# Performance work log

Hardware: AMD Instinct MI355X
Metric: run time of the kernel (lower is better)

Reference implementation:

```python
import jax, jax.numpy as jnp
import numpy as np

B, T, D = 32, 2000, 512
L_ORDER, R_ORDER = 20, 20
L_STRIDE, R_STRIDE = 2, 2
LPAD = L_ORDER * L_STRIDE  # 40
RPAD = R_ORDER * R_STRIDE  # 40


def setup_inputs() -> dict:
    key = jax.random.key(0)
    k1, k2 = jax.random.split(key)
    x = jax.random.normal(k1, (B, T, D), dtype=jnp.float32)
    filt = jax.random.normal(k2, (L_ORDER + R_ORDER + 1, D), dtype=jnp.float32)
    return {"x": x, "filt": filt}


def _fsmn(x, filt):
    # x: [B, T, D], filt: [L_ORDER + R_ORDER + 1, D]
    t = x.shape[1]
    xp = jnp.pad(x, ((0, 0), (LPAD, RPAD), (0, 0)))
    # Center of output frame t sits at padded index t + LPAD.
    # Left tap i hits padded offset t + i*L_STRIDE  (i = 0..L_ORDER-1),
    # i.e. signal offset -(L_ORDER - i)*L_STRIDE relative to the frame.
    out = xp[:, LPAD:LPAD + t] * filt[L_ORDER]  # center tap
    for i in range(L_ORDER):
        s = i * L_STRIDE
        out = out + xp[:, s:s + t] * filt[i]
    # Right tap j hits signal offset 1 + j*R_STRIDE (matches x[f+1 : f+1+R*rs : rs]).
    for j in range(R_ORDER):
        s = LPAD + 1 + j * R_STRIDE
        out = out + xp[:, s:s + t] * filt[L_ORDER + 1 + j]
    return out


def reference(x, filt):
    return _fsmn(x, filt)
```

## Files before the change

### kernel.cpp

```cpp
#include <hip/hip_runtime.h>


#define B_ 32
#define T_ 2000
#define D_ 512
#define S_ 1000
#define M_ 4

#define FOFF 0
#define XOFF (41 * 256)
#define LDS_FLOATS (XOFF + 64 * 256)

__device__ __forceinline__ float4 zf4() {
    float4 z; z.x = 0.f; z.y = 0.f; z.z = 0.f; z.w = 0.f; return z;
}

__device__ __forceinline__ void fma4(float4& a, const float4 f, const float4 w) {
    a.x = fmaf(f.x, w.x, a.x);
    a.y = fmaf(f.y, w.y, a.y);
    a.z = fmaf(f.z, w.z, a.z);
    a.w = fmaf(f.w, w.w, a.w);
}

__device__ __forceinline__ void gload_lds16(const float* g, float* l) {
    __builtin_amdgcn_global_load_lds(
        (const __attribute__((address_space(1))) void*)g,
        (__attribute__((address_space(3))) void*)l,
        16, 0, 0);
}

template<bool CHK>
__device__ __forceinline__ void fsmn_body(float* __restrict__ lds,
                                          const float* __restrict__ xb,
                                          const float* __restrict__ fb,
                                          float* __restrict__ ob,
                                          int m0, int R0, int lane, int mg)
{
    auto stageX = [&](int br) {
        float* l = lds + XOFF + ((br & 63) << 8);
        const int xr = R0 + br;
        if (!CHK || (unsigned)xr < (unsigned)T_) {
            gload_lds16(xb + (size_t)xr * D_, l);
        } else {
            *(float4*)(l + lane * 4) = zf4();
        }
    };
    auto stageF = [&](int fr) {
        gload_lds16(fb + (size_t)fr * D_, lds + FOFF + (fr << 8));
    };
    auto ldrow = [&](int br) -> float4 {
        return *(const float4*)(lds + XOFF + ((br & 63) << 8) + lane * 4);
    };
    auto ldsF = [&](int t) -> float4 {
        return *(const float4*)(lds + FOFF + (t << 8) + lane * 4);
    };

#pragma unroll
    for (int r = 0; r < 11; ++r) {
        const int fr = 4 * r + mg;
        if (fr <= 40) stageF(fr);
    }
#pragma unroll
    for (int r = 0; r < 12; ++r) stageX(4 * r + mg);
    __syncthreads();

    float4 wE[M_], wO[M_], ae[M_], ao[M_];
#pragma unroll
    for (int m = 0; m < M_; ++m) {
        wE[m] = ldrow(8 * mg + 2 * m);
        wO[m] = ldrow(8 * mg + 2 * m + 1);
        ae[m] = zf4(); ao[m] = zf4();
    }
    float4 qF0 = ldsF(0), qF1 = ldsF(1);

    auto dostep = [&](int t) {
        const float4 fv = qF0;
        qF0 = qF1;
        qF1 = (t + 2 <= 40) ? ldsF(t + 2) : zf4();
        if (t <= 20) {
#pragma unroll
            for (int m = 0; m < M_; ++m) { fma4(ae[m], fv, wE[m]); fma4(ao[m], fv, wO[m]); }
        } else {
#pragma unroll
            for (int m = 0; m < M_; ++m) { fma4(ao[m], fv, wE[m]); fma4(ae[m], fv, wO[m]); }
        }
        if (t < 40) {
#pragma unroll
            for (int m = 0; m < M_ - 1; ++m) wE[m] = wE[m + 1];
            wE[M_ - 1] = ldrow(8 * mg + 2 * t + 8);
            if (t != 20) {
#pragma unroll
                for (int m = 0; m < M_ - 1; ++m) wO[m] = wO[m + 1];
                wO[M_ - 1] = ldrow(8 * mg + 2 * t + 8 + ((t < 20) ? 1 : -1));
            }
        }
    };

#pragma unroll
    for (int p = 0; p < 5; ++p) {
        if (p <= 3) {
#pragma unroll
            for (int r = 0; r < 4; ++r) stageX(16 * (p + 3) + 4 * r + mg);
        }
#pragma unroll
        for (int t = 8 * p; t < ((p == 4) ? 41 : 8 * p + 8); ++t) dostep(t);
        if (p < 4) __syncthreads();
    }

#pragma unroll
    for (int m = 0; m < M_; ++m) {
        if (!CHK || (m0 + m) < S_) {
            *(float4*)(ob + (size_t)(2 * (m0 + m))     * D_) = ae[m];
            *(float4*)(ob + (size_t)(2 * (m0 + m) + 1) * D_) = ao[m];
        }
    }
}

__global__ __launch_bounds__(256, 1) void fsmn_kernel(
    const float* __restrict__ x, const float* __restrict__ filt,
    float* __restrict__ out)
{
    __shared__ float lds[LDS_FLOATS];

    const int lane = threadIdx.x;
    const int mg   = threadIdx.y;

    const int bid  = blockIdx.x;
    const int xcd  = bid & 7;
    const int slot = bid >> 3;
    const int n    = xcd * 504 + slot;
    const int mb   = n % 63;
    const int rest = n / 63;
    const int dh   = rest & 1;
    const int b    = rest >> 1;

    const int m0b = mb * 16;
    const int m0  = m0b + mg * M_;
    const int d   = (dh * 64 + lane) * 4;
    const float* xb = x + (size_t)b * T_ * D_ + d;
    const float* fb = filt + d;
    float*       ob = out + (size_t)b * T_ * D_ + d;
    const int R0  = 2 * m0b - 40;

    if (mb >= 2 && mb <= 60) fsmn_body<false>(lds, xb, fb, ob, m0, R0, lane, mg);
    else                     fsmn_body<true >(lds, xb, fb, ob, m0, R0, lane, mg);
}

extern "C" void kernel_launch(void* const* d_in, const int* in_sizes, int n_in,
                              void* d_out, int out_size, void* d_ws, size_t ws_size,
                              hipStream_t stream) {
    const float* x    = (const float*)d_in[0];
    const float* filt = (const float*)d_in[1];
    float*       out  = (float*)d_out;

    dim3 block(64, 4, 1);
    dim3 grid(4032, 1, 1);
    hipLaunchKernelGGL(fsmn_kernel, grid, block, 0, stream, x, filt, out);
}
```

Baseline: 276.2 us.

## Make blocks persistent over time segments with a circular LDS row buffer

Replaces the grid of 4032 short blocks, which each reloaded the filter and a 40-row halo, with 256 blocks. Each block loops over 16 tiles of a 256-step time segment and keeps input rows in a 112-row circular LDS ring. Filter taps are staged once per block, the halo is reused across tiles, and the next tile's rows are prefetched mid-compute. The cost is only 256 blocks on a 256-CU device with one block per CU, so there is less latency hiding, plus extra syncs and wrap arithmetic inside the loop.

```diff
diff --git a/kernel.cpp b/kernel.cpp
--- a/kernel.cpp
+++ b/kernel.cpp
@@ -6,10 +6,13 @@
 #define D_ 512
 #define S_ 1000
 #define M_ 4
-
+#define TM 16
+#define TILES 16
+#define SEGM (TM * TILES)
+#define XR 112
 #define FOFF 0
 #define XOFF (41 * 256)
-#define LDS_FLOATS (XOFF + 64 * 256)
+#define LDS_FLOATS (XOFF + XR * 256)
 
 __device__ __forceinline__ float4 zf4() {
     float4 z; z.x = 0.f; z.y = 0.f; z.z = 0.f; z.w = 0.f; return z;
@@ -29,93 +32,6 @@
         16, 0, 0);
 }
 
-template<bool CHK>
-__device__ __forceinline__ void fsmn_body(float* __restrict__ lds,
-                                          const float* __restrict__ xb,
-                                          const float* __restrict__ fb,
-                                          float* __restrict__ ob,
-                                          int m0, int R0, int lane, int mg)
-{
-    auto stageX = [&](int br) {
-        float* l = lds + XOFF + ((br & 63) << 8);
-        const int xr = R0 + br;
-        if (!CHK || (unsigned)xr < (unsigned)T_) {
-            gload_lds16(xb + (size_t)xr * D_, l);
-        } else {
-            *(float4*)(l + lane * 4) = zf4();
-        }
-    };
-    auto stageF = [&](int fr) {
-        gload_lds16(fb + (size_t)fr * D_, lds + FOFF + (fr << 8));
-    };
-    auto ldrow = [&](int br) -> float4 {
-        return *(const float4*)(lds + XOFF + ((br & 63) << 8) + lane * 4);
-    };
-    auto ldsF = [&](int t) -> float4 {
-        return *(const float4*)(lds + FOFF + (t << 8) + lane * 4);
-    };
-
-#pragma unroll
-    for (int r = 0; r < 11; ++r) {
-        const int fr = 4 * r + mg;
-        if (fr <= 40) stageF(fr);
-    }
-#pragma unroll
-    for (int r = 0; r < 12; ++r) stageX(4 * r + mg);
-    __syncthreads();
-
-    float4 wE[M_], wO[M_], ae[M_], ao[M_];
-#pragma unroll
-    for (int m = 0; m < M_; ++m) {
-        wE[m] = ldrow(8 * mg + 2 * m);
-        wO[m] = ldrow(8 * mg + 2 * m + 1);
-        ae[m] = zf4(); ao[m] = zf4();
-    }
-    float4 qF0 = ldsF(0), qF1 = ldsF(1);
-
-    auto dostep = [&](int t) {
-        const float4 fv = qF0;
-        qF0 = qF1;
-        qF1 = (t + 2 <= 40) ? ldsF(t + 2) : zf4();
-        if (t <= 20) {
-#pragma unroll
-            for (int m = 0; m < M_; ++m) { fma4(ae[m], fv, wE[m]); fma4(ao[m], fv, wO[m]); }
-        } else {
-#pragma unroll
-            for (int m = 0; m < M_; ++m) { fma4(ao[m], fv, wE[m]); fma4(ae[m], fv, wO[m]); }
-        }
-        if (t < 40) {
-#pragma unroll
-            for (int m = 0; m < M_ - 1; ++m) wE[m] = wE[m + 1];
-            wE[M_ - 1] = ldrow(8 * mg + 2 * t + 8);
-            if (t != 20) {
-#pragma unroll
-                for (int m = 0; m < M_ - 1; ++m) wO[m] = wO[m + 1];
-                wO[M_ - 1] = ldrow(8 * mg + 2 * t + 8 + ((t < 20) ? 1 : -1));
-            }
-        }
-    };
-
-#pragma unroll
-    for (int p = 0; p < 5; ++p) {
-        if (p <= 3) {
-#pragma unroll
-            for (int r = 0; r < 4; ++r) stageX(16 * (p + 3) + 4 * r + mg);
-        }
-#pragma unroll
-        for (int t = 8 * p; t < ((p == 4) ? 41 : 8 * p + 8); ++t) dostep(t);
-        if (p < 4) __syncthreads();
-    }
-
-#pragma unroll
-    for (int m = 0; m < M_; ++m) {
-        if (!CHK || (m0 + m) < S_) {
-            *(float4*)(ob + (size_t)(2 * (m0 + m))     * D_) = ae[m];
-            *(float4*)(ob + (size_t)(2 * (m0 + m) + 1) * D_) = ao[m];
-        }
-    }
-}
-
 __global__ __launch_bounds__(256, 1) void fsmn_kernel(
     const float* __restrict__ x, const float* __restrict__ filt,
     float* __restrict__ out)
@@ -126,24 +42,110 @@
     const int mg   = threadIdx.y;
 
     const int bid  = blockIdx.x;
-    const int xcd  = bid & 7;
-    const int slot = bid >> 3;
-    const int n    = xcd * 504 + slot;
-    const int mb   = n % 63;
-    const int rest = n / 63;
-    const int dh   = rest & 1;
-    const int b    = rest >> 1;
+    const int n    = (bid & 7) * 32 + (bid >> 3);
+    const int seg  = n & 3;
+    const int dh   = (n >> 2) & 1;
+    const int b    = n >> 3;
 
-    const int m0b = mb * 16;
-    const int m0  = m0b + mg * M_;
-    const int d   = (dh * 64 + lane) * 4;
+    const int m0seg = seg * SEGM;
+    const int d  = (dh * 64 + lane) * 4;
     const float* xb = x + (size_t)b * T_ * D_ + d;
     const float* fb = filt + d;
     float*       ob = out + (size_t)b * T_ * D_ + d;
-    const int R0  = 2 * m0b - 40;
+    const int R00 = 2 * m0seg - 40;
 
-    if (mb >= 2 && mb <= 60) fsmn_body<false>(lds, xb, fb, ob, m0, R0, lane, mg);
-    else                     fsmn_body<true >(lds, xb, fb, ob, m0, R0, lane, mg);
+    auto stageRow = [&](int absrow, int slot) {
+        float* l = lds + XOFF + (slot << 8);
+        if ((unsigned)absrow < (unsigned)T_) {
+            gload_lds16(xb + (size_t)absrow * D_, l);
+        } else {
+            *(float4*)(l + lane * 4) = zf4();
+        }
+    };
+    auto ldslot = [&](int slot) -> float4 {
+        return *(const float4*)(lds + XOFF + (slot << 8) + lane * 4);
+    };
+    auto ldsF = [&](int t) -> float4 {
+        return *(const float4*)(lds + FOFF + (t << 8) + lane * 4);
+    };
+    auto wrap = [](int s) { return s >= XR ? s - XR : s; };
+
+#pragma unroll
+    for (int i = 0; i < 11; ++i) {
+        const int fr = 4 * i + mg;
+        if (fr <= 40) gload_lds16(fb + (size_t)fr * D_, lds + FOFF + (fr << 8));
+    }
+#pragma unroll
+    for (int i = 0; i < 28; ++i) {
+        const int r = 4 * i + mg;
+        stageRow(R00 + r, r);
+    }
+    __syncthreads();
+
+    int tbm = 0;
+    int m0k = m0seg;
+#pragma unroll 1
+    for (int k = 0; k < TILES; ++k) {
+        const int wb  = tbm + 8 * mg;
+        const int m0w = m0k + M_ * mg;
+
+        float4 wE[M_], wO[M_], ae[M_], ao[M_];
+#pragma unroll
+        for (int m = 0; m < M_; ++m) {
+            wE[m] = ldslot(wrap(wb + 2 * m));
+            wO[m] = ldslot(wrap(wb + 2 * m + 1));
+            ae[m] = zf4(); ao[m] = zf4();
+        }
+        float4 qF0 = ldsF(0), qF1 = ldsF(1);
+
+        auto dostep = [&](int t) {
+            const float4 fv = qF0;
+            qF0 = qF1;
+            qF1 = (t + 2 <= 40) ? ldsF(t + 2) : zf4();
+            if (t <= 20) {
+#pragma unroll
+                for (int m = 0; m < M_; ++m) { fma4(ae[m], fv, wE[m]); fma4(ao[m], fv, wO[m]); }
+            } else {
+#pragma unroll
+                for (int m = 0; m < M_; ++m) { fma4(ao[m], fv, wE[m]); fma4(ae[m], fv, wO[m]); }
+            }
+            if (t < 40) {
+#pragma unroll
+                for (int m = 0; m < M_ - 1; ++m) wE[m] = wE[m + 1];
+                wE[M_ - 1] = ldslot(wrap(wb + 2 * t + 8));
+                if (t != 20) {
+#pragma unroll
+                    for (int m = 0; m < M_ - 1; ++m) wO[m] = wO[m + 1];
+                    wO[M_ - 1] = ldslot(wrap(wb + 2 * t + 8 + ((t < 20) ? 1 : -1)));
+                }
+            }
+        };
+
+#pragma unroll
+        for (int t = 0; t < 12; ++t) dostep(t);
+        __syncthreads();
+
+        if (k < TILES - 1) {
+            const int absbase = R00 + 32 * k + 112 + 8 * mg;
+#pragma unroll
+            for (int i = 0; i < 8; ++i) stageRow(absbase + i, wrap(wb + i));
+        }
+
+#pragma unroll
+        for (int t = 12; t <= 40; ++t) dostep(t);
+
+#pragma unroll
+        for (int m = 0; m < M_; ++m) {
+            if (m0w + m < S_) {
+                *(float4*)(ob + (size_t)(2 * (m0w + m))     * D_) = ae[m];
+                *(float4*)(ob + (size_t)(2 * (m0w + m) + 1) * D_) = ao[m];
+            }
+        }
+        __syncthreads();
+
+        tbm += 32; if (tbm >= XR) tbm -= XR;
+        m0k += TM;
+    }
 }
 
 extern "C" void kernel_launch(void* const* d_in, const int* in_sizes, int n_in,
@@ -154,6 +156,6 @@
     float*       out  = (float*)d_out;
 
     dim3 block(64, 4, 1);
-    dim3 grid(4032, 1, 1);
+    dim3 grid(256, 1, 1);
     hipLaunchKernelGGL(fsmn_kernel, grid, block, 0, stream, x, filt, out);
 }
```

After: 812.5 us. 2.94x slower.

## Enlarge per-block time tile to 24 output pairs and stream filter rows through a ring

Applied to the files above, without the earlier changes.

Each warp-row now computes 6 output pairs instead of 4, so a block covers 24 output pairs and the grid shrinks to 2688 blocks. The larger tile cuts the halo overhead of re-reading the 80 padding rows per block and amortizes the filter loads. Filter taps now sit in a 24-row LDS ring that is refilled alongside the x rows in the pipelined phases, keeping LDS usage bounded. Costs are more accumulator and window registers per thread and a larger x staging buffer, which may affect occupancy and latency hiding.

```diff
diff --git a/kernel.cpp b/kernel.cpp
--- a/kernel.cpp
+++ b/kernel.cpp
@@ -5,11 +5,12 @@
 #define T_ 2000
 #define D_ 512
 #define S_ 1000
-#define M_ 4
-
+#define M_ 6
+#define TM 24
+#define FRG 24
 #define FOFF 0
-#define XOFF (41 * 256)
-#define LDS_FLOATS (XOFF + 64 * 256)
+#define XOFF (FRG * 256)
+#define LDS_FLOATS (XOFF + 128 * 256)
 
 __device__ __forceinline__ float4 zf4() {
     float4 z; z.x = 0.f; z.y = 0.f; z.z = 0.f; z.w = 0.f; return z;
@@ -34,49 +35,46 @@
                                           const float* __restrict__ xb,
                                           const float* __restrict__ fb,
                                           float* __restrict__ ob,
-                                          int m0, int R0, int lane, int mg)
+                                          int m0w, int R0, int lane, int mg)
 {
-    auto stageX = [&](int br) {
-        float* l = lds + XOFF + ((br & 63) << 8);
-        const int xr = R0 + br;
-        if (!CHK || (unsigned)xr < (unsigned)T_) {
-            gload_lds16(xb + (size_t)xr * D_, l);
-        } else {
+    auto stgX = [&](int rel) {
+        float* l = lds + XOFF + (rel << 8);
+        const int row = R0 + rel;
+        if (!CHK || (unsigned)row < (unsigned)T_)
+            gload_lds16(xb + (size_t)row * D_, l);
+        else
             *(float4*)(l + lane * 4) = zf4();
-        }
     };
-    auto stageF = [&](int fr) {
-        gload_lds16(fb + (size_t)fr * D_, lds + FOFF + (fr << 8));
+    auto stgF = [&](int fr) {
+        if (fr <= 40)
+            gload_lds16(fb + (size_t)fr * D_, lds + FOFF + ((fr % FRG) << 8));
     };
-    auto ldrow = [&](int br) -> float4 {
-        return *(const float4*)(lds + XOFF + ((br & 63) << 8) + lane * 4);
+    auto ldrow = [&](int rel) -> float4 {
+        return *(const float4*)(lds + XOFF + (rel << 8) + lane * 4);
     };
-    auto ldsF = [&](int t) -> float4 {
-        return *(const float4*)(lds + FOFF + (t << 8) + lane * 4);
+    auto ldF = [&](int t) -> float4 {
+        return *(const float4*)(lds + FOFF + ((t % FRG) << 8) + lane * 4);
     };
 
 #pragma unroll
-    for (int r = 0; r < 11; ++r) {
-        const int fr = 4 * r + mg;
-        if (fr <= 40) stageF(fr);
-    }
+    for (int i = 0; i < 16; ++i) stgX(4 * i + mg);
 #pragma unroll
-    for (int r = 0; r < 12; ++r) stageX(4 * r + mg);
+    for (int i = 0; i < 4; ++i) stgF(4 * mg + i);
     __syncthreads();
 
     float4 wE[M_], wO[M_], ae[M_], ao[M_];
 #pragma unroll
     for (int m = 0; m < M_; ++m) {
-        wE[m] = ldrow(8 * mg + 2 * m);
-        wO[m] = ldrow(8 * mg + 2 * m + 1);
+        wE[m] = ldrow(12 * mg + 2 * m);
+        wO[m] = ldrow(12 * mg + 2 * m + 1);
         ae[m] = zf4(); ao[m] = zf4();
     }
-    float4 qF0 = ldsF(0), qF1 = ldsF(1);
+    float4 qF0 = ldF(0), qF1 = ldF(1);
 
     auto dostep = [&](int t) {
         const float4 fv = qF0;
         qF0 = qF1;
-        qF1 = (t + 2 <= 40) ? ldsF(t + 2) : zf4();
+        qF1 = (t + 2 <= 40) ? ldF(t + 2) : zf4();
         if (t <= 20) {
 #pragma unroll
             for (int m = 0; m < M_; ++m) { fma4(ae[m], fv, wE[m]); fma4(ao[m], fv, wO[m]); }
@@ -87,11 +85,11 @@
         if (t < 40) {
 #pragma unroll
             for (int m = 0; m < M_ - 1; ++m) wE[m] = wE[m + 1];
-            wE[M_ - 1] = ldrow(8 * mg + 2 * t + 8);
+            wE[M_ - 1] = ldrow(12 * mg + 2 * t + 12);
             if (t != 20) {
 #pragma unroll
                 for (int m = 0; m < M_ - 1; ++m) wO[m] = wO[m + 1];
-                wO[M_ - 1] = ldrow(8 * mg + 2 * t + 8 + ((t < 20) ? 1 : -1));
+                wO[M_ - 1] = ldrow(12 * mg + 2 * t + 12 + ((t < 20) ? 1 : -1));
             }
         }
     };
@@ -100,7 +98,10 @@
     for (int p = 0; p < 5; ++p) {
         if (p <= 3) {
 #pragma unroll
-            for (int r = 0; r < 4; ++r) stageX(16 * (p + 3) + 4 * r + mg);
+            for (int i = 0; i < 4; ++i)
+                stgX(16 * (p + 4) + 4 * mg + i);
+            stgF(8 * (p + 2) + 2 * mg);
+            stgF(8 * (p + 2) + 2 * mg + 1);
         }
 #pragma unroll
         for (int t = 8 * p; t < ((p == 4) ? 41 : 8 * p + 8); ++t) dostep(t);
@@ -109,9 +110,9 @@
 
 #pragma unroll
     for (int m = 0; m < M_; ++m) {
-        if (!CHK || (m0 + m) < S_) {
-            *(float4*)(ob + (size_t)(2 * (m0 + m))     * D_) = ae[m];
-            *(float4*)(ob + (size_t)(2 * (m0 + m) + 1) * D_) = ao[m];
+        if (!CHK || (m0w + m) < S_) {
+            *(float4*)(ob + (size_t)(2 * (m0w + m))     * D_) = ae[m];
+            *(float4*)(ob + (size_t)(2 * (m0w + m) + 1) * D_) = ao[m];
         }
     }
 }
@@ -128,22 +129,22 @@
     const int bid  = blockIdx.x;
     const int xcd  = bid & 7;
     const int slot = bid >> 3;
-    const int n    = xcd * 504 + slot;
-    const int mb   = n % 63;
-    const int rest = n / 63;
+    const int n    = xcd * 336 + slot;
+    const int mb   = n % 42;
+    const int rest = n / 42;
     const int dh   = rest & 1;
     const int b    = rest >> 1;
 
-    const int m0b = mb * 16;
-    const int m0  = m0b + mg * M_;
+    const int m0b = mb * TM;
+    const int m0w = m0b + mg * M_;
     const int d   = (dh * 64 + lane) * 4;
     const float* xb = x + (size_t)b * T_ * D_ + d;
     const float* fb = filt + d;
     float*       ob = out + (size_t)b * T_ * D_ + d;
     const int R0  = 2 * m0b - 40;
 
-    if (mb >= 2 && mb <= 60) fsmn_body<false>(lds, xb, fb, ob, m0, R0, lane, mg);
-    else                     fsmn_body<true >(lds, xb, fb, ob, m0, R0, lane, mg);
+    if (mb >= 1 && mb <= 39) fsmn_body<false>(lds, xb, fb, ob, m0w, R0, lane, mg);
+    else                     fsmn_body<true >(lds, xb, fb, ob, m0w, R0, lane, mg);
 }
 
 extern "C" void kernel_launch(void* const* d_in, const int* in_sizes, int n_in,
@@ -154,6 +155,6 @@
     float*       out  = (float*)d_out;
 
     dim3 block(64, 4, 1);
-    dim3 grid(4032, 1, 1);
+    dim3 grid(2688, 1, 1);
     hipLaunchKernelGGL(fsmn_kernel, grid, block, 0, stream, x, filt, out);
 }
```

Result: slower. 287.2 us (+4.0%).
